# Optimization experiments

Measured on AMD Instinct MI355X. Metric: run time of the kernel, lower is better.

Reference implementation:

```python
import jax, jax.numpy as jnp
import numpy as np

B, T, C, H = 8, 2048, 1024, 128  # batch, seq (=block_size), n_embd, head_size


def setup_inputs() -> dict:
    key = jax.random.key(0)
    kx, kk, kq, kv = jax.random.split(key, 4)
    x = jax.random.normal(kx, (B, T, C), dtype=jnp.float32)
    # nn.Linear(n_embd, head_size, bias=False) weights, stored as (in, out) for x @ W
    s = 1.0 / np.sqrt(C)
    Wk = jax.random.normal(kk, (C, H), dtype=jnp.float32) * s
    Wq = jax.random.normal(kq, (C, H), dtype=jnp.float32) * s
    Wv = jax.random.normal(kv, (C, H), dtype=jnp.float32) * s
    return {"x": x, "Wk": Wk, "Wq": Wq, "Wv": Wv}


def reference(x, Wk, Wq, Wv):
    # x: [B, T, C]
    Bx, Tx, Cx = x.shape
    k = x @ Wk  # [B, T, H]
    q = x @ Wq  # [B, T, H]
    v = x @ Wv  # [B, T, H]
    # NOTE: source multiplies by C**0.5 (not 1/sqrt), kept faithfully
    wei = jnp.einsum("bth,bsh->bts", q, k) * (Cx ** 0.5)  # [B, T, T]
    causal = jnp.tril(jnp.ones((Tx, Tx), dtype=bool))
    wei = jnp.where(causal, wei, -jnp.inf)
    wei = jax.nn.softmax(wei, axis=-1)
    # dropout omitted (eval-mode reference)
    return wei @ v  # [B, T, H]
```

## Files before the change

### kernel.cpp

```cpp
#include <hip/hip_runtime.h>

constexpr int kB = 8;
constexpr int kT = 2048;
constexpr int kC = 1024;
constexpr int kH = 128;
constexpr int kM = kB * kT;
constexpr size_t kMH = (size_t)kM * kH;
constexpr size_t kWH = (size_t)kC * kH;

typedef __attribute__((ext_vector_type(8))) short bf16x8;
typedef __attribute__((ext_vector_type(4))) float f32x4;


__device__ inline unsigned short f2bf_rne(float f) {
    union { float f; unsigned int u; } x; x.f = f;
    unsigned int r = x.u + 0x7fff + ((x.u >> 16) & 1);
    return (unsigned short)(r >> 16);
}
__device__ inline float bf2f(unsigned short h) {
    union { float f; unsigned int u; } x; x.u = ((unsigned int)h) << 16;
    return x.f;
}
__device__ inline unsigned int pack_hi2(float a, float b) {
    return __builtin_amdgcn_perm(__float_as_uint(b), __float_as_uint(a),
                                 0x07060302u);
}
__device__ inline float hi_part(float v) {
    return __uint_as_float(__float_as_uint(v) & 0xffff0000u);
}
__device__ inline void load_lds16(const unsigned short* g, unsigned short* l) {
    __builtin_amdgcn_global_load_lds(
        (const __attribute__((address_space(1))) unsigned int*)g,
        (__attribute__((address_space(3))) unsigned int*)l, 16, 0, 0);
}

__global__ __launch_bounds__(256) void prep_w(
    const float* __restrict__ Wk, const float* __restrict__ Wq,
    const float* __restrict__ Wv, unsigned short* __restrict__ ws)
{
    const int h = blockIdx.x;
    const int mat = blockIdx.y;
    const float* W = (mat == 0) ? Wq : (mat == 1) ? Wk : Wv;
    unsigned short* hi = ws + 5 * kMH + (size_t)(mat * 2) * kWH;
    unsigned short* lo = hi + kWH;

    const int k0 = threadIdx.x * 4;
    unsigned short hv[4], lv[4];
#pragma unroll
    for (int j = 0; j < 4; ++j) {
        const float f = W[(size_t)(k0 + j) * kH + h];
        hv[j] = f2bf_rne(f);
        lv[j] = f2bf_rne(f - bf2f(hv[j]));
    }
    *(uint2*)&hi[(size_t)h * kC + k0] =
        make_uint2(((unsigned)hv[1] << 16) | hv[0], ((unsigned)hv[3] << 16) | hv[2]);
    *(uint2*)&lo[(size_t)h * kC + k0] =
        make_uint2(((unsigned)lv[1] << 16) | lv[0], ((unsigned)lv[3] << 16) | lv[2]);
}

__global__ __launch_bounds__(256) void qkv_mfma(
    const float* __restrict__ x, unsigned short* __restrict__ ws)
{
    __shared__ __align__(16) unsigned short Ah[64][36];
    __shared__ __align__(16) unsigned short Al[64][36];
    __shared__ __align__(16) unsigned short Bh[128 * 32];
    __shared__ __align__(16) unsigned short Bl[128 * 32];

    const int idx = blockIdx.x;
    const int mat = idx >> 8;
    const int m0 = (idx & 255) * 64;
    const unsigned short* wThi = ws + 5 * kMH + (size_t)(mat * 2) * kWH;
    const unsigned short* wTlo = wThi + kWH;

    const int tid = threadIdx.x;
    const int w = tid >> 6, lane = tid & 63;
    const int li = lane & 15, quad = lane >> 4;
    const int wm = w >> 1, wn = w & 1;

    const int ar = tid >> 2;
    const int ac = (tid & 3) * 8;

    f32x4 acc[2][4];
#pragma unroll
    for (int i = 0; i < 2; ++i)
#pragma unroll
        for (int j = 0; j < 4; ++j) acc[i][j] = (f32x4){0.f, 0.f, 0.f, 0.f};

    if (mat <= 1) {
        for (int kt = 0; kt < kC; kt += 32) {
            if (kt) __syncthreads();
            {
                const float4 x0 = *(const float4*)(x + (size_t)(m0 + ar) * kC + kt + ac);
                const float4 x1 = *(const float4*)(x + (size_t)(m0 + ar) * kC + kt + ac + 4);
                *(uint2*)&Ah[ar][ac] = make_uint2(pack_hi2(x0.x, x0.y), pack_hi2(x0.z, x0.w));
                *(uint2*)&Ah[ar][ac + 4] = make_uint2(pack_hi2(x1.x, x1.y), pack_hi2(x1.z, x1.w));
                const float l0 = x0.x - hi_part(x0.x), l1 = x0.y - hi_part(x0.y);
                const float l2 = x0.z - hi_part(x0.z), l3 = x0.w - hi_part(x0.w);
                const float l4 = x1.x - hi_part(x1.x), l5 = x1.y - hi_part(x1.y);
                const float l6 = x1.z - hi_part(x1.z), l7 = x1.w - hi_part(x1.w);
                *(uint2*)&Al[ar][ac] = make_uint2(pack_hi2(l0, l1), pack_hi2(l2, l3));
                *(uint2*)&Al[ar][ac + 4] = make_uint2(pack_hi2(l4, l5), pack_hi2(l6, l7));
            }
#pragma unroll
            for (int u = 0; u < 2; ++u) {
                const int f = u * 256 + tid;
                const int row = f >> 2, g = (f & 3) ^ ((f >> 2) & 3);
                load_lds16(wThi + (size_t)row * kC + kt + g * 8, Bh + f * 8);
                load_lds16(wTlo + (size_t)row * kC + kt + g * 8, Bl + f * 8);
            }
            __syncthreads();

            bf16x8 ah[2], al[2];
#pragma unroll
            for (int mt = 0; mt < 2; ++mt) {
                ah[mt] = *(const bf16x8*)&Ah[wm * 32 + mt * 16 + li][quad * 8];
                al[mt] = *(const bf16x8*)&Al[wm * 32 + mt * 16 + li][quad * 8];
            }
#pragma unroll
            for (int nt = 0; nt < 4; ++nt) {
                const int row = wn * 64 + nt * 16 + li;
                const int pos = quad ^ (row & 3);
                const bf16x8 bh = *(const bf16x8*)&Bh[row * 32 + pos * 8];
                const bf16x8 bl = *(const bf16x8*)&Bl[row * 32 + pos * 8];
#pragma unroll
                for (int mt = 0; mt < 2; ++mt) {
                    acc[mt][nt] = __builtin_amdgcn_mfma_f32_16x16x32_bf16(ah[mt], bh, acc[mt][nt], 0, 0, 0);
                    acc[mt][nt] = __builtin_amdgcn_mfma_f32_16x16x32_bf16(al[mt], bh, acc[mt][nt], 0, 0, 0);
                    acc[mt][nt] = __builtin_amdgcn_mfma_f32_16x16x32_bf16(ah[mt], bl, acc[mt][nt], 0, 0, 0);
                }
            }
        }
        unsigned short* hip_ = ws + (size_t)(mat * 2) * kMH;
        unsigned short* lop  = hip_ + kMH;
        const float sc = (mat == 0) ? 32.0f : 1.0f;
#pragma unroll
        for (int mt = 0; mt < 2; ++mt)
#pragma unroll
            for (int nt = 0; nt < 4; ++nt) {
                const int col = wn * 64 + nt * 16 + li;
#pragma unroll
                for (int reg = 0; reg < 4; ++reg) {
                    const int row = m0 + wm * 32 + mt * 16 + quad * 4 + reg;
                    const float v = acc[mt][nt][reg] * sc;
                    hip_[(size_t)row * kH + col] = (unsigned short)(__float_as_uint(v) >> 16);
                    lop[(size_t)row * kH + col] =
                        (unsigned short)(__float_as_uint(v - hi_part(v)) >> 16);
                }
            }
    } else {
        for (int kt = 0; kt < kC; kt += 32) {
            if (kt) __syncthreads();
            {
                const float4 x0 = *(const float4*)(x + (size_t)(m0 + ar) * kC + kt + ac);
                const float4 x1 = *(const float4*)(x + (size_t)(m0 + ar) * kC + kt + ac + 4);
                unsigned short h0 = f2bf_rne(x0.x), h1 = f2bf_rne(x0.y);
                unsigned short h2 = f2bf_rne(x0.z), h3 = f2bf_rne(x0.w);
                unsigned short h4 = f2bf_rne(x1.x), h5 = f2bf_rne(x1.y);
                unsigned short h6 = f2bf_rne(x1.z), h7 = f2bf_rne(x1.w);
                *(uint2*)&Ah[ar][ac] =
                    make_uint2(((unsigned)h1 << 16) | h0, ((unsigned)h3 << 16) | h2);
                *(uint2*)&Ah[ar][ac + 4] =
                    make_uint2(((unsigned)h5 << 16) | h4, ((unsigned)h7 << 16) | h6);
            }
#pragma unroll
            for (int u = 0; u < 2; ++u) {
                const int f = u * 256 + tid;
                const int row = f >> 2, g = (f & 3) ^ ((f >> 2) & 3);
                load_lds16(wThi + (size_t)row * kC + kt + g * 8, Bh + f * 8);
            }
            __syncthreads();

            bf16x8 a[2];
#pragma unroll
            for (int mt = 0; mt < 2; ++mt)
                a[mt] = *(const bf16x8*)&Ah[wm * 32 + mt * 16 + li][quad * 8];
#pragma unroll
            for (int nt = 0; nt < 4; ++nt) {
                const int row = wn * 64 + nt * 16 + li;
                const int pos = quad ^ (row & 3);
                const bf16x8 bh = *(const bf16x8*)&Bh[row * 32 + pos * 8];
#pragma unroll
                for (int mt = 0; mt < 2; ++mt)
                    acc[mt][nt] = __builtin_amdgcn_mfma_f32_16x16x32_bf16(a[mt], bh, acc[mt][nt], 0, 0, 0);
            }
        }
        unsigned short* vt = ws + 4 * kMH;
        const int bb = m0 >> 11;
        const int t00 = (m0 & (kT - 1)) + wm * 32;
#pragma unroll
        for (int mt = 0; mt < 2; ++mt)
#pragma unroll
            for (int nt = 0; nt < 4; ++nt) {
                const int h = wn * 64 + nt * 16 + li;
                ushort4 pk;
                pk.x = f2bf_rne(acc[mt][nt][0]);
                pk.y = f2bf_rne(acc[mt][nt][1]);
                pk.z = f2bf_rne(acc[mt][nt][2]);
                pk.w = f2bf_rne(acc[mt][nt][3]);
                const int t0 = t00 + mt * 16 + quad * 4;
                *(ushort4*)&vt[((size_t)(bb * kH + h)) * kT + t0] = pk;
            }
    }
}

__global__ __launch_bounds__(256, 2) void attn_mfma(
    const unsigned short* __restrict__ ws, float* __restrict__ out)
{
    __shared__ __align__(16) unsigned short Ps[4][2][16][40];
    __shared__ __align__(16) float Ml[4][32][2];
    __shared__ __align__(16) float Obuf[3][32][128];

    const int tid = threadIdx.x;
    const int w = tid >> 6, lane = tid & 63;
    const int li = lane & 15, quad = lane >> 4;

    const int idx = blockIdx.x;
    const int b = idx & 7;
    const int j = idx >> 3;
    const int qt = (j < 32) ? j : 95 - j;
    const int i0 = qt * 32;
    const int nc = qt + 1;

    const unsigned short* qhi = ws;
    const unsigned short* qlo = ws + kMH;
    const unsigned short* khi = ws + 2 * kMH;
    const unsigned short* klo = ws + 3 * kMH;
    const unsigned short* vt  = ws + 4 * kMH;

    bf16x8 qh[2][4], ql[2][4];
#pragma unroll
    for (int mi = 0; mi < 2; ++mi) {
        const size_t qoff = ((size_t)(b * kT + i0 + mi * 16 + li)) * kH;
#pragma unroll
        for (int kc = 0; kc < 4; ++kc) {
            qh[mi][kc] = *(const bf16x8*)(qhi + qoff + kc * 32 + quad * 8);
            ql[mi][kc] = *(const bf16x8*)(qlo + qoff + kc * 32 + quad * 8);
        }
    }

    f32x4 o[2][8];
#pragma unroll
    for (int mi = 0; mi < 2; ++mi)
#pragma unroll
        for (int ht = 0; ht < 8; ++ht) o[mi][ht] = (f32x4){0.f, 0.f, 0.f, 0.f};
    float m_i[2][4], l_i[2][4];
#pragma unroll
    for (int mi = 0; mi < 2; ++mi)
#pragma unroll
        for (int reg = 0; reg < 4; ++reg) { m_i[mi][reg] = -3.0e38f; l_i[mi][reg] = 0.f; }

    for (int jc = w; jc < nc; jc += 4) {
        const int t0 = jc * 32;
        bf16x8 vf[8];
#pragma unroll
        for (int ht = 0; ht < 8; ++ht)
            vf[ht] = *(const bf16x8*)(vt + (size_t)(b * kH + ht * 16 + li) * kT +
                                      t0 + quad * 8);
        f32x4 s[2][2];
#pragma unroll
        for (int mi = 0; mi < 2; ++mi)
#pragma unroll
            for (int nt = 0; nt < 2; ++nt) s[mi][nt] = (f32x4){0.f, 0.f, 0.f, 0.f};
#pragma unroll
        for (int kc = 0; kc < 4; ++kc) {
            bf16x8 kh[2], kl[2];
#pragma unroll
            for (int nt = 0; nt < 2; ++nt) {
                const size_t ka =
                    ((size_t)(b * kT + t0 + nt * 16 + li)) * kH + kc * 32 + quad * 8;
                kh[nt] = *(const bf16x8*)(khi + ka);
                kl[nt] = *(const bf16x8*)(klo + ka);
            }
#pragma unroll
            for (int mi = 0; mi < 2; ++mi)
#pragma unroll
                for (int nt = 0; nt < 2; ++nt) {
                    s[mi][nt] = __builtin_amdgcn_mfma_f32_16x16x32_bf16(qh[mi][kc], kh[nt], s[mi][nt], 0, 0, 0);
                    s[mi][nt] = __builtin_amdgcn_mfma_f32_16x16x32_bf16(ql[mi][kc], kh[nt], s[mi][nt], 0, 0, 0);
                    s[mi][nt] = __builtin_amdgcn_mfma_f32_16x16x32_bf16(qh[mi][kc], kl[nt], s[mi][nt], 0, 0, 0);
                }
        }
        if (jc == qt) {
#pragma unroll
            for (int mi = 0; mi < 2; ++mi) {
                const int grow0 = i0 + mi * 16 + quad * 4;
#pragma unroll
                for (int nt = 0; nt < 2; ++nt) {
                    const int gcol = t0 + nt * 16 + li;
#pragma unroll
                    for (int reg = 0; reg < 4; ++reg)
                        if (gcol > grow0 + reg) s[mi][nt][reg] = -3.0e38f;
                }
            }
        }
#pragma unroll
        for (int mi = 0; mi < 2; ++mi) {
            float alpha[4];
#pragma unroll
            for (int reg = 0; reg < 4; ++reg) {
                float mr = fmaxf(s[mi][0][reg], s[mi][1][reg]);
                mr = fmaxf(mr, __shfl_xor(mr, 1));
                mr = fmaxf(mr, __shfl_xor(mr, 2));
                mr = fmaxf(mr, __shfl_xor(mr, 4));
                mr = fmaxf(mr, __shfl_xor(mr, 8));
                const float mn = fmaxf(m_i[mi][reg], mr);
                alpha[reg] = __expf(m_i[mi][reg] - mn);
                m_i[mi][reg] = mn;
                const float p0 = __expf(s[mi][0][reg] - mn);
                const float p1 = __expf(s[mi][1][reg] - mn);
                s[mi][0][reg] = p0; s[mi][1][reg] = p1;
                float rs = p0 + p1;
                rs += __shfl_xor(rs, 1);
                rs += __shfl_xor(rs, 2);
                rs += __shfl_xor(rs, 4);
                rs += __shfl_xor(rs, 8);
                l_i[mi][reg] = l_i[mi][reg] * alpha[reg] + rs;
            }
            const f32x4 av = {alpha[0], alpha[1], alpha[2], alpha[3]};
#pragma unroll
            for (int ht = 0; ht < 8; ++ht) o[mi][ht] *= av;
#pragma unroll
            for (int nt = 0; nt < 2; ++nt)
#pragma unroll
                for (int reg = 0; reg < 4; ++reg)
                    Ps[w][mi][quad * 4 + reg][nt * 16 + li] = f2bf_rne(s[mi][nt][reg]);
        }
#pragma unroll
        for (int mi = 0; mi < 2; ++mi) {
            const bf16x8 pf = *(const bf16x8*)&Ps[w][mi][li][quad * 8];
#pragma unroll
            for (int ht = 0; ht < 8; ++ht)
                o[mi][ht] = __builtin_amdgcn_mfma_f32_16x16x32_bf16(pf, vf[ht], o[mi][ht], 0, 0, 0);
        }
    }

    if (li == 0) {
#pragma unroll
        for (int mi = 0; mi < 2; ++mi)
#pragma unroll
            for (int reg = 0; reg < 4; ++reg) {
                Ml[w][mi * 16 + quad * 4 + reg][0] = m_i[mi][reg];
                Ml[w][mi * 16 + quad * 4 + reg][1] = l_i[mi][reg];
            }
    }
    __syncthreads();
    float a_self[2][4], linv[2][4];
#pragma unroll
    for (int mi = 0; mi < 2; ++mi)
#pragma unroll
        for (int reg = 0; reg < 4; ++reg) {
            const int row = mi * 16 + quad * 4 + reg;
            const float m0_ = Ml[0][row][0], m1 = Ml[1][row][0];
            const float m2 = Ml[2][row][0], m3 = Ml[3][row][0];
            const float ms = fmaxf(fmaxf(m0_, m1), fmaxf(m2, m3));
            const float L = Ml[0][row][1] * __expf(m0_ - ms) +
                            Ml[1][row][1] * __expf(m1 - ms) +
                            Ml[2][row][1] * __expf(m2 - ms) +
                            Ml[3][row][1] * __expf(m3 - ms);
            a_self[mi][reg] = __expf(m_i[mi][reg] - ms);
            linv[mi][reg] = 1.0f / L;
        }
    if (w) {
#pragma unroll
        for (int mi = 0; mi < 2; ++mi)
#pragma unroll
            for (int ht = 0; ht < 8; ++ht)
#pragma unroll
                for (int reg = 0; reg < 4; ++reg)
                    Obuf[w - 1][mi * 16 + quad * 4 + reg][ht * 16 + li] =
                        o[mi][ht][reg] * a_self[mi][reg];
    }
    __syncthreads();
    if (w == 0) {
#pragma unroll
        for (int mi = 0; mi < 2; ++mi)
#pragma unroll
            for (int ht = 0; ht < 8; ++ht)
#pragma unroll
                for (int reg = 0; reg < 4; ++reg) {
                    const int row = mi * 16 + quad * 4 + reg;
                    const int col = ht * 16 + li;
                    const float v = o[mi][ht][reg] * a_self[mi][reg] +
                                    Obuf[0][row][col] + Obuf[1][row][col] +
                                    Obuf[2][row][col];
                    out[(size_t)(b * kT + i0 + row) * kH + col] = v * linv[mi][reg];
                }
    }
}

extern "C" void kernel_launch(void* const* d_in, const int* in_sizes, int n_in,
                              void* d_out, int out_size, void* d_ws, size_t ws_size,
                              hipStream_t stream) {
    const float* x  = (const float*)d_in[0];
    const float* Wk = (const float*)d_in[1];
    const float* Wq = (const float*)d_in[2];
    const float* Wv = (const float*)d_in[3];
    unsigned short* ws = (unsigned short*)d_ws;
    float* out = (float*)d_out;

    hipLaunchKernelGGL(prep_w, dim3(128, 3), dim3(256), 0, stream, Wk, Wq, Wv, ws);
    hipLaunchKernelGGL(qkv_mfma, dim3(768), dim3(256), 0, stream, x, ws);
    hipLaunchKernelGGL(attn_mfma, dim3(512), dim3(256), 0, stream,
                       (const unsigned short*)ws, out);
}
```

Before: 199.2 us.

## Load x directly into registers in QKV GEMM and use exp2 softmax

```diff
diff --git a/kernel.cpp b/kernel.cpp
--- a/kernel.cpp
+++ b/kernel.cpp
@@ -7,6 +7,8 @@
 constexpr int kM = kB * kT;
 constexpr size_t kMH = (size_t)kM * kH;
 constexpr size_t kWH = (size_t)kC * kH;
+
+#define QSCALE 46.166241308446828f
 
 typedef __attribute__((ext_vector_type(8))) short bf16x8;
 typedef __attribute__((ext_vector_type(4))) float f32x4;
@@ -61,10 +63,8 @@
 __global__ __launch_bounds__(256) void qkv_mfma(
     const float* __restrict__ x, unsigned short* __restrict__ ws)
 {
-    __shared__ __align__(16) unsigned short Ah[64][36];
-    __shared__ __align__(16) unsigned short Al[64][36];
-    __shared__ __align__(16) unsigned short Bh[128 * 32];
-    __shared__ __align__(16) unsigned short Bl[128 * 32];
+    __shared__ __align__(16) unsigned short Bh[128 * 64];
+    __shared__ __align__(16) unsigned short Bl[128 * 64];
 
     const int idx = blockIdx.x;
     const int mat = idx >> 8;
@@ -75,131 +75,114 @@
     const int tid = threadIdx.x;
     const int w = tid >> 6, lane = tid & 63;
     const int li = lane & 15, quad = lane >> 4;
-    const int wm = w >> 1, wn = w & 1;
-
-    const int ar = tid >> 2;
-    const int ac = (tid & 3) * 8;
-
-    f32x4 acc[2][4];
-#pragma unroll
-    for (int i = 0; i < 2; ++i)
-#pragma unroll
-        for (int j = 0; j < 4; ++j) acc[i][j] = (f32x4){0.f, 0.f, 0.f, 0.f};
+
+    const float* xrow = x + (size_t)(m0 + w * 16 + li) * kC;
+
+    f32x4 acc[8];
+#pragma unroll
+    for (int j = 0; j < 8; ++j) acc[j] = (f32x4){0.f, 0.f, 0.f, 0.f};
+
+    for (int kt = 0; kt < kC; kt += 64) {
+        if (kt) __syncthreads();
+#pragma unroll
+        for (int u = 0; u < 4; ++u) {
+            const int f = u * 256 + tid;
+            const int row = f >> 3, g = (f & 7) ^ (row & 7);
+            load_lds16(wThi + (size_t)row * kC + kt + g * 8, Bh + f * 8);
+            if (mat <= 1)
+                load_lds16(wTlo + (size_t)row * kC + kt + g * 8, Bl + f * 8);
+        }
+        float4 xa[2][2];
+#pragma unroll
+        for (int kc = 0; kc < 2; ++kc) {
+            xa[kc][0] = *(const float4*)(xrow + kt + kc * 32 + quad * 8);
+            xa[kc][1] = *(const float4*)(xrow + kt + kc * 32 + quad * 8 + 4);
+        }
+        bf16x8 ah[2], al[2];
+        if (mat <= 1) {
+#pragma unroll
+            for (int kc = 0; kc < 2; ++kc) {
+                const float4 a0 = xa[kc][0], a1 = xa[kc][1];
+                unsigned int hp[4], lp[4];
+                hp[0] = pack_hi2(a0.x, a0.y); hp[1] = pack_hi2(a0.z, a0.w);
+                hp[2] = pack_hi2(a1.x, a1.y); hp[3] = pack_hi2(a1.z, a1.w);
+                lp[0] = pack_hi2(a0.x - hi_part(a0.x), a0.y - hi_part(a0.y));
+                lp[1] = pack_hi2(a0.z - hi_part(a0.z), a0.w - hi_part(a0.w));
+                lp[2] = pack_hi2(a1.x - hi_part(a1.x), a1.y - hi_part(a1.y));
+                lp[3] = pack_hi2(a1.z - hi_part(a1.z), a1.w - hi_part(a1.w));
+                ah[kc] = *(bf16x8*)hp;
+                al[kc] = *(bf16x8*)lp;
+            }
+        } else {
+#pragma unroll
+            for (int kc = 0; kc < 2; ++kc) {
+                const float4 a0 = xa[kc][0], a1 = xa[kc][1];
+                unsigned short e[8];
+                e[0] = f2bf_rne(a0.x); e[1] = f2bf_rne(a0.y);
+                e[2] = f2bf_rne(a0.z); e[3] = f2bf_rne(a0.w);
+                e[4] = f2bf_rne(a1.x); e[5] = f2bf_rne(a1.y);
+                e[6] = f2bf_rne(a1.z); e[7] = f2bf_rne(a1.w);
+                ah[kc] = *(bf16x8*)e;
+            }
+        }
+        __syncthreads();
+
+        if (mat <= 1) {
+#pragma unroll
+            for (int kc = 0; kc < 2; ++kc)
+#pragma unroll
+                for (int nt = 0; nt < 8; ++nt) {
+                    const int row = nt * 16 + li;
+                    const int pos = (kc * 4 + quad) ^ (row & 7);
+                    const bf16x8 bh = *(const bf16x8*)&Bh[row * 64 + pos * 8];
+                    const bf16x8 bl = *(const bf16x8*)&Bl[row * 64 + pos * 8];
+                    acc[nt] = __builtin_amdgcn_mfma_f32_16x16x32_bf16(ah[kc], bh, acc[nt], 0, 0, 0);
+                    acc[nt] = __builtin_amdgcn_mfma_f32_16x16x32_bf16(al[kc], bh, acc[nt], 0, 0, 0);
+                    acc[nt] = __builtin_amdgcn_mfma_f32_16x16x32_bf16(ah[kc], bl, acc[nt], 0, 0, 0);
+                }
+        } else {
+#pragma unroll
+            for (int kc = 0; kc < 2; ++kc)
+#pragma unroll
+                for (int nt = 0; nt < 8; ++nt) {
+                    const int row = nt * 16 + li;
+                    const int pos = (kc * 4 + quad) ^ (row & 7);
+                    const bf16x8 bh = *(const bf16x8*)&Bh[row * 64 + pos * 8];
+                    acc[nt] = __builtin_amdgcn_mfma_f32_16x16x32_bf16(ah[kc], bh, acc[nt], 0, 0, 0);
+                }
+        }
+    }
 
     if (mat <= 1) {
-        for (int kt = 0; kt < kC; kt += 32) {
-            if (kt) __syncthreads();
-            {
-                const float4 x0 = *(const float4*)(x + (size_t)(m0 + ar) * kC + kt + ac);
-                const float4 x1 = *(const float4*)(x + (size_t)(m0 + ar) * kC + kt + ac + 4);
-                *(uint2*)&Ah[ar][ac] = make_uint2(pack_hi2(x0.x, x0.y), pack_hi2(x0.z, x0.w));
-                *(uint2*)&Ah[ar][ac + 4] = make_uint2(pack_hi2(x1.x, x1.y), pack_hi2(x1.z, x1.w));
-                const float l0 = x0.x - hi_part(x0.x), l1 = x0.y - hi_part(x0.y);
-                const float l2 = x0.z - hi_part(x0.z), l3 = x0.w - hi_part(x0.w);
-                const float l4 = x1.x - hi_part(x1.x), l5 = x1.y - hi_part(x1.y);
-                const float l6 = x1.z - hi_part(x1.z), l7 = x1.w - hi_part(x1.w);
-                *(uint2*)&Al[ar][ac] = make_uint2(pack_hi2(l0, l1), pack_hi2(l2, l3));
-                *(uint2*)&Al[ar][ac + 4] = make_uint2(pack_hi2(l4, l5), pack_hi2(l6, l7));
-            }
-#pragma unroll
-            for (int u = 0; u < 2; ++u) {
-                const int f = u * 256 + tid;
-                const int row = f >> 2, g = (f & 3) ^ ((f >> 2) & 3);
-                load_lds16(wThi + (size_t)row * kC + kt + g * 8, Bh + f * 8);
-                load_lds16(wTlo + (size_t)row * kC + kt + g * 8, Bl + f * 8);
-            }
-            __syncthreads();
-
-            bf16x8 ah[2], al[2];
-#pragma unroll
-            for (int mt = 0; mt < 2; ++mt) {
-                ah[mt] = *(const bf16x8*)&Ah[wm * 32 + mt * 16 + li][quad * 8];
-                al[mt] = *(const bf16x8*)&Al[wm * 32 + mt * 16 + li][quad * 8];
-            }
-#pragma unroll
-            for (int nt = 0; nt < 4; ++nt) {
-                const int row = wn * 64 + nt * 16 + li;
-                const int pos = quad ^ (row & 3);
-                const bf16x8 bh = *(const bf16x8*)&Bh[row * 32 + pos * 8];
-                const bf16x8 bl = *(const bf16x8*)&Bl[row * 32 + pos * 8];
-#pragma unroll
-                for (int mt = 0; mt < 2; ++mt) {
-                    acc[mt][nt] = __builtin_amdgcn_mfma_f32_16x16x32_bf16(ah[mt], bh, acc[mt][nt], 0, 0, 0);
-                    acc[mt][nt] = __builtin_amdgcn_mfma_f32_16x16x32_bf16(al[mt], bh, acc[mt][nt], 0, 0, 0);
-                    acc[mt][nt] = __builtin_amdgcn_mfma_f32_16x16x32_bf16(ah[mt], bl, acc[mt][nt], 0, 0, 0);
-                }
-            }
-        }
         unsigned short* hip_ = ws + (size_t)(mat * 2) * kMH;
         unsigned short* lop  = hip_ + kMH;
-        const float sc = (mat == 0) ? 32.0f : 1.0f;
-#pragma unroll
-        for (int mt = 0; mt < 2; ++mt)
-#pragma unroll
-            for (int nt = 0; nt < 4; ++nt) {
-                const int col = wn * 64 + nt * 16 + li;
-#pragma unroll
-                for (int reg = 0; reg < 4; ++reg) {
-                    const int row = m0 + wm * 32 + mt * 16 + quad * 4 + reg;
-                    const float v = acc[mt][nt][reg] * sc;
-                    hip_[(size_t)row * kH + col] = (unsigned short)(__float_as_uint(v) >> 16);
-                    lop[(size_t)row * kH + col] =
-                        (unsigned short)(__float_as_uint(v - hi_part(v)) >> 16);
-                }
-            }
+        const float sc = (mat == 0) ? QSCALE : 1.0f;
+#pragma unroll
+        for (int nt = 0; nt < 8; ++nt) {
+            const int col = nt * 16 + li;
+#pragma unroll
+            for (int reg = 0; reg < 4; ++reg) {
+                const int row = m0 + w * 16 + quad * 4 + reg;
+                const float v = acc[nt][reg] * sc;
+                hip_[(size_t)row * kH + col] = (unsigned short)(__float_as_uint(v) >> 16);
+                lop[(size_t)row * kH + col] =
+                    (unsigned short)(__float_as_uint(v - hi_part(v)) >> 16);
+            }
+        }
     } else {
-        for (int kt = 0; kt < kC; kt += 32) {
-            if (kt) __syncthreads();
-            {
-                const float4 x0 = *(const float4*)(x + (size_t)(m0 + ar) * kC + kt + ac);
-                const float4 x1 = *(const float4*)(x + (size_t)(m0 + ar) * kC + kt + ac + 4);
-                unsigned short h0 = f2bf_rne(x0.x), h1 = f2bf_rne(x0.y);
-                unsigned short h2 = f2bf_rne(x0.z), h3 = f2bf_rne(x0.w);
-                unsigned short h4 = f2bf_rne(x1.x), h5 = f2bf_rne(x1.y);
-                unsigned short h6 = f2bf_rne(x1.z), h7 = f2bf_rne(x1.w);
-                *(uint2*)&Ah[ar][ac] =
-                    make_uint2(((unsigned)h1 << 16) | h0, ((unsigned)h3 << 16) | h2);
-                *(uint2*)&Ah[ar][ac + 4] =
-                    make_uint2(((unsigned)h5 << 16) | h4, ((unsigned)h7 << 16) | h6);
-            }
-#pragma unroll
-            for (int u = 0; u < 2; ++u) {
-                const int f = u * 256 + tid;
-                const int row = f >> 2, g = (f & 3) ^ ((f >> 2) & 3);
-                load_lds16(wThi + (size_t)row * kC + kt + g * 8, Bh + f * 8);
-            }
-            __syncthreads();
-
-            bf16x8 a[2];
-#pragma unroll
-            for (int mt = 0; mt < 2; ++mt)
-                a[mt] = *(const bf16x8*)&Ah[wm * 32 + mt * 16 + li][quad * 8];
-#pragma unroll
-            for (int nt = 0; nt < 4; ++nt) {
-                const int row = wn * 64 + nt * 16 + li;
-                const int pos = quad ^ (row & 3);
-                const bf16x8 bh = *(const bf16x8*)&Bh[row * 32 + pos * 8];
-#pragma unroll
-                for (int mt = 0; mt < 2; ++mt)
-                    acc[mt][nt] = __builtin_amdgcn_mfma_f32_16x16x32_bf16(a[mt], bh, acc[mt][nt], 0, 0, 0);
-            }
-        }
         unsigned short* vt = ws + 4 * kMH;
         const int bb = m0 >> 11;
-        const int t00 = (m0 & (kT - 1)) + wm * 32;
-#pragma unroll
-        for (int mt = 0; mt < 2; ++mt)
-#pragma unroll
-            for (int nt = 0; nt < 4; ++nt) {
-                const int h = wn * 64 + nt * 16 + li;
-                ushort4 pk;
-                pk.x = f2bf_rne(acc[mt][nt][0]);
-                pk.y = f2bf_rne(acc[mt][nt][1]);
-                pk.z = f2bf_rne(acc[mt][nt][2]);
-                pk.w = f2bf_rne(acc[mt][nt][3]);
-                const int t0 = t00 + mt * 16 + quad * 4;
-                *(ushort4*)&vt[((size_t)(bb * kH + h)) * kT + t0] = pk;
-            }
+        const int t0 = (m0 & (kT - 1)) + w * 16 + quad * 4;
+#pragma unroll
+        for (int nt = 0; nt < 8; ++nt) {
+            const int h = nt * 16 + li;
+            ushort4 pk;
+            pk.x = f2bf_rne(acc[nt][0]);
+            pk.y = f2bf_rne(acc[nt][1]);
+            pk.z = f2bf_rne(acc[nt][2]);
+            pk.w = f2bf_rne(acc[nt][3]);
+            *(ushort4*)&vt[((size_t)(bb * kH + h)) * kT + t0] = pk;
+        }
     }
 }
 
@@ -304,10 +287,10 @@
                 mr = fmaxf(mr, __shfl_xor(mr, 4));
                 mr = fmaxf(mr, __shfl_xor(mr, 8));
                 const float mn = fmaxf(m_i[mi][reg], mr);
-                alpha[reg] = __expf(m_i[mi][reg] - mn);
+                alpha[reg] = exp2f(m_i[mi][reg] - mn);
                 m_i[mi][reg] = mn;
-                const float p0 = __expf(s[mi][0][reg] - mn);
-                const float p1 = __expf(s[mi][1][reg] - mn);
+                const float p0 = exp2f(s[mi][0][reg] - mn);
+                const float p1 = exp2f(s[mi][1][reg] - mn);
                 s[mi][0][reg] = p0; s[mi][1][reg] = p1;
                 float rs = p0 + p1;
                 rs += __shfl_xor(rs, 1);
@@ -353,11 +336,11 @@
             const float m0_ = Ml[0][row][0], m1 = Ml[1][row][0];
             const float m2 = Ml[2][row][0], m3 = Ml[3][row][0];
             const float ms = fmaxf(fmaxf(m0_, m1), fmaxf(m2, m3));
-            const float L = Ml[0][row][1] * __expf(m0_ - ms) +
-                            Ml[1][row][1] * __expf(m1 - ms) +
-                            Ml[2][row][1] * __expf(m2 - ms) +
-                            Ml[3][row][1] * __expf(m3 - ms);
-            a_self[mi][reg] = __expf(m_i[mi][reg] - ms);
+            const float L = Ml[0][row][1] * exp2f(m0_ - ms) +
+                            Ml[1][row][1] * exp2f(m1 - ms) +
+                            Ml[2][row][1] * exp2f(m2 - ms) +
+                            Ml[3][row][1] * exp2f(m3 - ms);
+            a_self[mi][reg] = exp2f(m_i[mi][reg] - ms);
             linv[mi][reg] = 1.0f / L;
         }
     if (w) {
```

After: 195.5 us. No clear change (-1.9%).
